# Performance work log

Hardware: AMD Instinct MI355X
Metric: run time of the kernel (lower is better)

The kernel has to match this reference:

```python
import jax, jax.numpy as jnp
import numpy as np

N = 50000      # nodes
E = 800000     # edges
D = 128        # input feature dim
H = 8          # heads
C = 16         # out_channels per head (H*C == D, concat output width == D)
SLOPE = 0.2    # PyG GATConv leaky_relu negative slope


def gat_layer(x, src, dst, W, a_src, a_dst, b):
    # linear transform, shared for src/dst (PyG GATConv with int in_channels)
    h = (x @ W).reshape(N, H, C)                      # [N,H,C]
    alpha_src = jnp.einsum('nhc,hc->nh', h, a_src)    # [N,H]
    alpha_dst = jnp.einsum('nhc,hc->nh', h, a_dst)    # [N,H]
    e = jax.nn.leaky_relu(alpha_src[src] + alpha_dst[dst], SLOPE)  # [E,H]
    # segment softmax over edges grouped by destination node
    emax = jax.ops.segment_max(e, dst, num_segments=N)            # [N,H]
    emax = jnp.where(jnp.isfinite(emax), emax, 0.0)               # nodes with no in-edges
    ex = jnp.exp(e - emax[dst])                                   # [E,H]
    denom = jax.ops.segment_sum(ex, dst, num_segments=N)          # [N,H]
    alpha = ex / (denom[dst] + 1e-16)                             # [E,H]
    # weighted scatter-aggregate of source messages
    out = jax.ops.segment_sum(h[src] * alpha[:, :, None], dst, num_segments=N)  # [N,H,C]
    return out.reshape(N, H * C) + b, alpha


def setup_inputs() -> dict:
    key = jax.random.key(0)
    ks = jax.random.split(key, 10)
    s = 1.0 / np.sqrt(D)
    return {
        'x': jax.random.normal(ks[0], (N, D), dtype=jnp.float32),
        'W1': jax.random.normal(ks[1], (D, H * C), dtype=jnp.float32) * s,
        'a_src1': jax.random.normal(ks[2], (H, C), dtype=jnp.float32) * s,
        'a_dst1': jax.random.normal(ks[3], (H, C), dtype=jnp.float32) * s,
        'b1': jnp.zeros((H * C,), dtype=jnp.float32),
        'W2': jax.random.normal(ks[4], (H * C, H * C), dtype=jnp.float32) * s,
        'a_src2': jax.random.normal(ks[5], (H, C), dtype=jnp.float32) * s,
        'a_dst2': jax.random.normal(ks[6], (H, C), dtype=jnp.float32) * s,
        'b2': jnp.zeros((H * C,), dtype=jnp.float32),
        'edge_index': jax.random.randint(ks[7], (2, E), 0, N, dtype=jnp.int64),
    }


def reference(x, W1, a_src1, a_dst1, b1, W2, a_src2, a_dst2, b2, edge_index):
    src, dst = edge_index[0], edge_index[1]
    x1, alpha1 = gat_layer(x, src, dst, W1, a_src1, a_dst1, b1)
    x2, alpha2 = gat_layer(x1, src, dst, W2, a_src2, a_dst2, b2)
    # matches torch forward: (x, attention_weights per layer)
    return x2, alpha1, alpha2
```

## Files before the change

kernel.cpp:

```cpp
#include <hip/hip_runtime.h>
#include <hip/hip_fp16.h>

#define NN 50000
#define NE 800000
#define SLOPE 0.2f
#define SCAN_B 196
#define ECAP 64

typedef _Float16 half8 __attribute__((ext_vector_type(8)));
typedef float f32x4 __attribute__((ext_vector_type(4)));
typedef unsigned int u32x4 __attribute__((ext_vector_type(4)));

__device__ __forceinline__ float lrelu(float v) { return v >= 0.f ? v : SLOPE * v; }
__device__ __forceinline__ unsigned int f2u(float f) {
    unsigned int b = __float_as_uint(f);
    return (b & 0x80000000u) ? ~b : (b | 0x80000000u);
}
__device__ __forceinline__ float u2f(unsigned int u) {
    return __uint_as_float((u & 0x80000000u) ? (u & 0x7fffffffu) : ~u);
}

__global__ __launch_bounds__(256) void prep_all(
    const float* __restrict__ W1, const float* __restrict__ as1, const float* __restrict__ ad1,
    __half* __restrict__ WT1,
    const float* __restrict__ W2, const float* __restrict__ as2, const float* __restrict__ ad2,
    __half* __restrict__ WT2,
    int* __restrict__ counts, unsigned int* __restrict__ gm1, unsigned int* __restrict__ gm2)
{
    const int t0 = blockIdx.x * 256 + threadIdx.x;
    const int stride = gridDim.x * 256;
    for (int i = t0; i < NN; i += stride) counts[i] = 0;
    if (t0 < 8) { gm1[t0] = f2u(-1e30f); gm2[t0] = f2u(-1e30f); }
    #pragma unroll
    for (int layer = 0; layer < 2; ++layer) {
        const float* W = layer ? W2 : W1;
        const float* as_ = layer ? as2 : as1;
        const float* ad_ = layer ? ad2 : ad1;
        __half* WT = layer ? WT2 : WT1;
        for (int idx = t0; idx < 1024; idx += stride) {
            const int k = idx >> 3, h = idx & 7;
            float s1 = 0.f, s2 = 0.f;
            #pragma unroll
            for (int c = 0; c < 16; ++c) {
                const float w = W[k * 128 + h * 16 + c];
                s1 += w * as_[h * 16 + c];
                s2 += w * ad_[h * 16 + c];
            }
            WT[(size_t)(128 + h) * 128 + k] = (__half)s1;
            WT[(size_t)(136 + h) * 128 + k] = (__half)s2;
        }
        for (int idx = t0; idx < 16384; idx += stride) {
            const int k = idx >> 7, c = idx & 127;
            WT[(size_t)c * 128 + k] = (__half)W[idx];
        }
    }
}

template<bool F32IN>
__global__ __launch_bounds__(256) void mfma_gemm(
    const void* __restrict__ Xin, const __half* __restrict__ WT,
    __half* __restrict__ H16, float* __restrict__ asrc, float* __restrict__ adst,
    unsigned int* __restrict__ gmaxE)
{
    __shared__ __half WTs[144 * 136];
    __shared__ unsigned int smax[8];
    const int t = threadIdx.x;
    const int lane = t & 63;
    const int w = t >> 6;
    const int r16 = lane & 15;
    const int g = lane >> 4;
    const int rowStrip = blockIdx.x * 64 + w * 16;
    const int rowm = min(rowStrip + r16, NN - 1);

    #pragma unroll
    for (int k = 0; k < 9; ++k) {
        const int flat = (t + k * 256) * 8;
        const int row = flat >> 7, col = flat & 127;
        *(half8*)&WTs[row * 136 + col] = *(const half8*)&WT[flat];
    }
    if (t < 8) smax[t] = f2u(-1e30f);

    half8 afr[4];
    if constexpr (F32IN) {
        const float* xr = (const float*)Xin + (size_t)rowm * 128;
        #pragma unroll
        for (int ks = 0; ks < 4; ++ks) {
            const int k0 = ks * 32 + 8 * g;
            const float4 p = *(const float4*)&xr[k0];
            const float4 q = *(const float4*)&xr[k0 + 4];
            half8 a;
            a[0] = (_Float16)p.x; a[1] = (_Float16)p.y; a[2] = (_Float16)p.z; a[3] = (_Float16)p.w;
            a[4] = (_Float16)q.x; a[5] = (_Float16)q.y; a[6] = (_Float16)q.z; a[7] = (_Float16)q.w;
            afr[ks] = a;
        }
    } else {
        const __half* xr = (const __half*)Xin + (size_t)rowm * 128;
        #pragma unroll
        for (int ks = 0; ks < 4; ++ks) {
            afr[ks] = *(const half8*)&xr[ks * 32 + 8 * g];
        }
    }
    __syncthreads();

    for (int ct = 0; ct < 9; ++ct) {
        f32x4 acc = {0.f, 0.f, 0.f, 0.f};
        const __half* wrow = &WTs[(ct * 16 + r16) * 136 + 8 * g];
        #pragma unroll
        for (int ks = 0; ks < 4; ++ks) {
            const half8 b = *(const half8*)&wrow[ks * 32];
            acc = __builtin_amdgcn_mfma_f32_16x16x32_f16(afr[ks], b, acc, 0, 0, 0);
        }
        if (ct < 8) {
            #pragma unroll
            for (int rr = 0; rr < 4; ++rr) {
                const int r = rowStrip + 4 * g + rr;
                if (r < NN) H16[(size_t)r * 128 + ct * 16 + r16] = (__half)acc[rr];
            }
        } else {
            float lmax = fmaxf(fmaxf(acc[0], acc[1]), fmaxf(acc[2], acc[3]));
            #pragma unroll
            for (int rr = 0; rr < 4; ++rr) {
                const int r = rowStrip + 4 * g + rr;
                if (r < NN) {
                    if (r16 < 8) asrc[(size_t)r * 8 + r16] = acc[rr];
                    else         adst[(size_t)r * 8 + (r16 - 8)] = acc[rr];
                }
            }
            lmax = fmaxf(lmax, __shfl_xor(lmax, 16));
            lmax = fmaxf(lmax, __shfl_xor(lmax, 32));
            if (g == 0 && r16 < 8) atomicMax(&smax[r16], f2u(lmax));
        }
    }
    __syncthreads();
    if (t < 8) atomicMax(&gmaxE[t], smax[t]);
}

__global__ __launch_bounds__(256) void hist_rank(
    const int* __restrict__ dst, int* __restrict__ counts, int* __restrict__ rank) {
    int e = blockIdx.x * 256 + threadIdx.x;
    if (e >= NE) return;
    int d = dst[e];
    if ((unsigned)d >= NN) d = 0;
    rank[e] = atomicAdd(&counts[d], 1);
}

__global__ __launch_bounds__(256) void block_sum(const int* __restrict__ counts,
                                                 int* __restrict__ bsum) {
    __shared__ int red[256];
    int t = threadIdx.x, i = blockIdx.x * 256 + t;
    red[t] = (i < NN) ? counts[i] : 0;
    __syncthreads();
    for (int s = 128; s > 0; s >>= 1) {
        if (t < s) red[t] += red[t + s];
        __syncthreads();
    }
    if (t == 0) bsum[blockIdx.x] = red[0];
}

__global__ __launch_bounds__(256) void scan_bsum(const int* __restrict__ bsum,
                                                 int* __restrict__ boff) {
    __shared__ int sh[256];
    int t = threadIdx.x;
    int v = (t < SCAN_B) ? bsum[t] : 0;
    sh[t] = v;
    __syncthreads();
    for (int d = 1; d < 256; d <<= 1) {
        int u = (t >= d) ? sh[t - d] : 0;
        __syncthreads();
        sh[t] += u;
        __syncthreads();
    }
    if (t < SCAN_B) boff[t] = sh[t] - v;
}

__global__ __launch_bounds__(256) void scan_final(
    const int* __restrict__ counts, const int* __restrict__ boff,
    int* __restrict__ off)
{
    __shared__ int sh[256];
    int t = threadIdx.x, i = blockIdx.x * 256 + t;
    int v = (i < NN) ? counts[i] : 0;
    sh[t] = v;
    __syncthreads();
    for (int d = 1; d < 256; d <<= 1) {
        int u = (t >= d) ? sh[t - d] : 0;
        __syncthreads();
        sh[t] += u;
        __syncthreads();
    }
    if (i < NN) {
        int o = boff[blockIdx.x] + sh[t] - v;
        off[i] = o;
        if (i == NN - 1) off[NN] = o + v;
    }
}

__global__ __launch_bounds__(256) void place_csr(
    const int* __restrict__ src, const int* __restrict__ dst,
    const int* __restrict__ rank, const int* __restrict__ off,
    int2* __restrict__ csrES) {
    int e = blockIdx.x * 256 + threadIdx.x;
    if (e >= NE) return;
    int s = src[e], d = dst[e];
    if ((unsigned)s >= NN) s = 0;
    if ((unsigned)d >= NN) d = 0;
    int pos = off[d] + rank[e];
    unsigned long long v = ((unsigned long long)(unsigned)s << 32) | (unsigned)e;
    __builtin_nontemporal_store(v, (unsigned long long*)&csrES[pos]);
}

__device__ __forceinline__ void gather_fma(
    const __half* __restrict__ H16, int sk, int ql, float pm,
    float4& accA, float4& accB)
{
    float4 raw = *(const float4*)&H16[(size_t)sk * 128 + ql * 8];
    const __half2* ph = (const __half2*)&raw;
    const float2 f0 = __half22float2(ph[0]);
    const float2 f1 = __half22float2(ph[1]);
    const float2 f2 = __half22float2(ph[2]);
    const float2 f3 = __half22float2(ph[3]);
    accA.x = fmaf(f0.x, pm, accA.x);
    accA.y = fmaf(f0.y, pm, accA.y);
    accA.z = fmaf(f1.x, pm, accA.z);
    accA.w = fmaf(f1.y, pm, accA.w);
    accB.x = fmaf(f2.x, pm, accB.x);
    accB.y = fmaf(f2.y, pm, accB.y);
    accB.z = fmaf(f3.x, pm, accB.z);
    accB.w = fmaf(f3.y, pm, accB.w);
}

template<typename OT, bool NTOUT>
__global__ __launch_bounds__(256) void node_fused(
    const int* __restrict__ off, const int2* __restrict__ csrES,
    const float* __restrict__ asrc, const float* __restrict__ adst,
    const unsigned int* __restrict__ gmaxE,
    const __half* __restrict__ H16, const float* __restrict__ bias,
    float* __restrict__ alpha, OT* __restrict__ out)
{
    __shared__ float pcache[4][ECAP * 8];
    __shared__ int2  scache[4][ECAP];
    const int w = threadIdx.x >> 6;
    int wid = (blockIdx.x * 256 + threadIdx.x) >> 6;
    if (wid >= NN) return;
    const int lane = threadIdx.x & 63;
    const int n = wid;
    const int p0 = off[n], p1 = off[n + 1];
    const int deg = p1 - p0;
    const int h = lane & 7;
    const int el = lane >> 3;
    const float ad = adst[n * 8 + h];
    const float M = lrelu(u2f(gmaxE[h]) + ad);

    const int q  = lane >> 4;
    const int ql = lane & 15;
    const int hq = ql >> 1;

    float l = 0.f;
    float4 accA = make_float4(0.f, 0.f, 0.f, 0.f);
    float4 accB = make_float4(0.f, 0.f, 0.f, 0.f);

    if (deg > 0) {
        const int pEnd = p1 - 1;
        int2  es = csrES[min(p0 + el, pEnd)];
        float av = asrc[(size_t)es.y * 8 + h];
        for (int base = 0; base < deg; base += 8) {
            int2 es_nx = csrES[min(p0 + base + 8 + el, pEnd)];
            const int i = base + el;
            const int s = es.y;
            float p = 0.f;
            if (i < deg) {
                p = __expf(lrelu(av + ad) - M);
                l += p;
                if (i < ECAP) {
                    pcache[w][i * 8 + h] = p;
                    if (h == 0) scache[w][i] = es;
                }
            }
            const int cnt = min(8, deg - base);
            {
                const int kc = min(q, cnt - 1);
                const float pk = __shfl(p, kc * 8 + hq);
                const int   sk = __shfl(s, kc * 8);
                const float pm = (q < cnt) ? pk : 0.f;
                gather_fma(H16, sk, ql, pm, accA, accB);
            }
            if (cnt > 4) {
                const int kw = 4 + q;
                const int kc = min(kw, cnt - 1);
                const float pk = __shfl(p, kc * 8 + hq);
                const int   sk = __shfl(s, kc * 8);
                const float pm = (kw < cnt) ? pk : 0.f;
                gather_fma(H16, sk, ql, pm, accA, accB);
            }
            av = asrc[(size_t)es_nx.y * 8 + h];
            es = es_nx;
        }
    }
    l += __shfl_xor(l, 8);
    l += __shfl_xor(l, 16);
    l += __shfl_xor(l, 32);
    const float inv = 1.f / (l + 1e-16f);

    for (int i = el; i < deg && i < ECAP; i += 8) {
        int2 es = scache[w][i];
        __builtin_nontemporal_store(pcache[w][i * 8 + h] * inv,
                                    &alpha[(size_t)es.x * 8 + h]);
    }
    for (int i = ECAP + el; i < deg; i += 8) {
        int2 es = csrES[p0 + i];
        float v = lrelu(asrc[es.y * 8 + h] + ad);
        __builtin_nontemporal_store(__expf(v - M) * inv,
                                    &alpha[(size_t)es.x * 8 + h]);
    }

    const float invH = __shfl(inv, hq);
    accA.x += __shfl_xor(accA.x, 16); accA.x += __shfl_xor(accA.x, 32);
    accA.y += __shfl_xor(accA.y, 16); accA.y += __shfl_xor(accA.y, 32);
    accA.z += __shfl_xor(accA.z, 16); accA.z += __shfl_xor(accA.z, 32);
    accA.w += __shfl_xor(accA.w, 16); accA.w += __shfl_xor(accA.w, 32);
    accB.x += __shfl_xor(accB.x, 16); accB.x += __shfl_xor(accB.x, 32);
    accB.y += __shfl_xor(accB.y, 16); accB.y += __shfl_xor(accB.y, 32);
    accB.z += __shfl_xor(accB.z, 16); accB.z += __shfl_xor(accB.z, 32);
    accB.w += __shfl_xor(accB.w, 16); accB.w += __shfl_xor(accB.w, 32);
    if (q == 0) {
        const float4 bva = *(const float4*)&bias[ql * 8];
        const float4 bvb = *(const float4*)&bias[ql * 8 + 4];
        const float o0 = accA.x * invH + bva.x, o1 = accA.y * invH + bva.y;
        const float o2 = accA.z * invH + bva.z, o3 = accA.w * invH + bva.w;
        const float o4 = accB.x * invH + bvb.x, o5 = accB.y * invH + bvb.y;
        const float o6 = accB.z * invH + bvb.z, o7 = accB.w * invH + bvb.w;
        if constexpr (sizeof(OT) == 4) {
            if constexpr (NTOUT) {
                f32x4 oa = {o0, o1, o2, o3}, ob = {o4, o5, o6, o7};
                __builtin_nontemporal_store(oa, (f32x4*)&out[(size_t)n * 128 + ql * 8]);
                __builtin_nontemporal_store(ob, (f32x4*)&out[(size_t)n * 128 + ql * 8 + 4]);
            } else {
                float4 oa = {o0, o1, o2, o3}, ob = {o4, o5, o6, o7};
                *(float4*)&out[(size_t)n * 128 + ql * 8]     = oa;
                *(float4*)&out[(size_t)n * 128 + ql * 8 + 4] = ob;
            }
        } else {
            __half2 p0h = __floats2half2_rn(o0, o1);
            __half2 p1h = __floats2half2_rn(o2, o3);
            __half2 p2h = __floats2half2_rn(o4, o5);
            __half2 p3h = __floats2half2_rn(o6, o7);
            u32x4 pk = {*(unsigned*)&p0h, *(unsigned*)&p1h, *(unsigned*)&p2h, *(unsigned*)&p3h};
            if constexpr (NTOUT) {
                __builtin_nontemporal_store(pk, (u32x4*)&out[(size_t)n * 128 + ql * 8]);
            } else {
                *(u32x4*)&out[(size_t)n * 128 + ql * 8] = pk;
            }
        }
    }
}

extern "C" void kernel_launch(void* const* d_in, const int* in_sizes, int n_in,
                              void* d_out, int out_size, void* d_ws, size_t ws_size,
                              hipStream_t stream)
{
    const float* x   = (const float*)d_in[0];
    const float* W1  = (const float*)d_in[1];
    const float* as1 = (const float*)d_in[2];
    const float* ad1 = (const float*)d_in[3];
    const float* b1  = (const float*)d_in[4];
    const float* W2  = (const float*)d_in[5];
    const float* as2 = (const float*)d_in[6];
    const float* ad2 = (const float*)d_in[7];
    const float* b2  = (const float*)d_in[8];
    const int*   ei  = (const int*)d_in[9];
    const int* srcp = ei;
    const int* dstp = ei + NE;

    float* outx   = (float*)d_out;
    float* alpha1 = outx + (size_t)NN * 128;
    float* alpha2 = alpha1 + (size_t)NE * 8;

    __half* h16 = (__half*)d_ws;
    __half* x1h = h16 + (size_t)NN * 128;
    __half* wt1 = x1h + (size_t)NN * 128;
    __half* wt2 = wt1 + (size_t)144 * 128;
    float* asrc = (float*)(wt2 + (size_t)144 * 128);
    float* adst = asrc + (size_t)NN * 8;
    int* counts = (int*)(adst + (size_t)NN * 8);
    int* off    = counts + NN;
    int* rank   = off + NN + 1;
    int2* csrES = (int2*)(rank + NE);
    int* bsum   = (int*)(csrES + NE);
    int* boff   = bsum + SCAN_B;
    unsigned int* gm1 = (unsigned int*)(boff + SCAN_B);
    unsigned int* gm2 = gm1 + 8;

    int gemmGrid = (NN + 63) / 64;
    int nodeGrid = (NN + 3) / 4;
    int edgeGrid = (NE + 255) / 256;

    prep_all<<<SCAN_B, 256, 0, stream>>>(W1, as1, ad1, wt1, W2, as2, ad2, wt2, counts, gm1, gm2);
    hist_rank<<<edgeGrid, 256, 0, stream>>>(dstp, counts, rank);
    block_sum<<<SCAN_B, 256, 0, stream>>>(counts, bsum);
    scan_bsum<<<1, 256, 0, stream>>>(bsum, boff);
    scan_final<<<SCAN_B, 256, 0, stream>>>(counts, boff, off);
    place_csr<<<edgeGrid, 256, 0, stream>>>(srcp, dstp, rank, off, csrES);

    mfma_gemm<true><<<gemmGrid, 256, 0, stream>>>(x, wt1, h16, asrc, adst, gm1);
    node_fused<__half, false><<<nodeGrid, 256, 0, stream>>>(off, csrES, asrc, adst, gm1, h16, b1, alpha1, x1h);

    mfma_gemm<false><<<gemmGrid, 256, 0, stream>>>(x1h, wt2, h16, asrc, adst, gm2);
    node_fused<float, true><<<nodeGrid, 256, 0, stream>>>(off, csrES, asrc, adst, gm2, h16, b2, alpha2, outx);
}
```

Baseline: 215.2 us.

## Fuse CSR placement into first GEMM and unroll edge loop by sixteen

The separate place_csr kernel is removed, and its scatter of (src, edge) pairs into CSR order moves into the first MFMA GEMM kernel. Each GEMM block handles 1024 edges, loading them before the matrix work and storing them after it, which saves one launch and overlaps the scatter with compute. The node aggregation loop is also unrolled to process two groups of 8 edges per iteration, putting more independent gathers in flight. The cost is higher register pressure in both kernels. Coverage depends on the GEMM grid (782 blocks × 1024 edges) being large enough to cover all 800000 edges.

```diff
diff --git a/kernel.cpp b/kernel.cpp
--- a/kernel.cpp
+++ b/kernel.cpp
@@ -56,11 +56,14 @@
     }
 }
 
-template<bool F32IN>
+template<bool F32IN, bool DOPLACE>
 __global__ __launch_bounds__(256) void mfma_gemm(
     const void* __restrict__ Xin, const __half* __restrict__ WT,
     __half* __restrict__ H16, float* __restrict__ asrc, float* __restrict__ adst,
-    unsigned int* __restrict__ gmaxE)
+    unsigned int* __restrict__ gmaxE,
+    const int* __restrict__ srcA, const int* __restrict__ dstA,
+    const int* __restrict__ rank, const int* __restrict__ offA,
+    int2* __restrict__ csrES)
 {
     __shared__ __half WTs[144 * 136];
     __shared__ unsigned int smax[8];
@@ -79,6 +82,24 @@
         *(half8*)&WTs[row * 136 + col] = *(const half8*)&WT[flat];
     }
     if (t < 8) smax[t] = f2u(-1e30f);
+
+    int ppos[DOPLACE ? 4 : 1];
+    unsigned long long pval[DOPLACE ? 4 : 1];
+    if constexpr (DOPLACE) {
+        const int eBase = blockIdx.x * 1024;
+        #pragma unroll
+        for (int k = 0; k < 4; ++k) {
+            const int e = eBase + k * 256 + t;
+            ppos[k] = -1;
+            if (e < NE) {
+                int s = srcA[e], d = dstA[e];
+                if ((unsigned)s >= NN) s = 0;
+                if ((unsigned)d >= NN) d = 0;
+                ppos[k] = offA[d] + rank[e];
+                pval[k] = ((unsigned long long)(unsigned)s << 32) | (unsigned)e;
+            }
+        }
+    }
 
     half8 afr[4];
     if constexpr (F32IN) {
@@ -131,6 +152,15 @@
             if (g == 0 && r16 < 8) atomicMax(&smax[r16], f2u(lmax));
         }
     }
+
+    if constexpr (DOPLACE) {
+        #pragma unroll
+        for (int k = 0; k < 4; ++k) {
+            if (ppos[k] >= 0) {
+                __builtin_nontemporal_store(pval[k], (unsigned long long*)&csrES[ppos[k]]);
+            }
+        }
+    }
     __syncthreads();
     if (t < 8) atomicMax(&gmaxE[t], smax[t]);
 }
@@ -193,20 +223,6 @@
         off[i] = o;
         if (i == NN - 1) off[NN] = o + v;
     }
-}
-
-__global__ __launch_bounds__(256) void place_csr(
-    const int* __restrict__ src, const int* __restrict__ dst,
-    const int* __restrict__ rank, const int* __restrict__ off,
-    int2* __restrict__ csrES) {
-    int e = blockIdx.x * 256 + threadIdx.x;
-    if (e >= NE) return;
-    int s = src[e], d = dst[e];
-    if ((unsigned)s >= NN) s = 0;
-    if ((unsigned)d >= NN) d = 0;
-    int pos = off[d] + rank[e];
-    unsigned long long v = ((unsigned long long)(unsigned)s << 32) | (unsigned)e;
-    __builtin_nontemporal_store(v, (unsigned long long*)&csrES[pos]);
 }
 
 __device__ __forceinline__ void gather_fma(
@@ -261,39 +277,62 @@
 
     if (deg > 0) {
         const int pEnd = p1 - 1;
-        int2  es = csrES[min(p0 + el, pEnd)];
-        float av = asrc[(size_t)es.y * 8 + h];
-        for (int base = 0; base < deg; base += 8) {
-            int2 es_nx = csrES[min(p0 + base + 8 + el, pEnd)];
-            const int i = base + el;
-            const int s = es.y;
-            float p = 0.f;
-            if (i < deg) {
-                p = __expf(lrelu(av + ad) - M);
-                l += p;
-                if (i < ECAP) {
-                    pcache[w][i * 8 + h] = p;
-                    if (h == 0) scache[w][i] = es;
+        int2  esA = csrES[min(p0 + el, pEnd)];
+        int2  esB = csrES[min(p0 + 8 + el, pEnd)];
+        float avA = asrc[(size_t)esA.y * 8 + h];
+        float avB = asrc[(size_t)esB.y * 8 + h];
+        for (int base = 0; base < deg; base += 16) {
+            int2 esA_nx = csrES[min(p0 + base + 16 + el, pEnd)];
+            int2 esB_nx = csrES[min(p0 + base + 24 + el, pEnd)];
+            const int iA = base + el, iB = base + 8 + el;
+            const int sA = esA.y, sB = esB.y;
+            float pA = 0.f, pB = 0.f;
+            if (iA < deg) {
+                pA = __expf(lrelu(avA + ad) - M);
+                l += pA;
+                if (iA < ECAP) {
+                    pcache[w][iA * 8 + h] = pA;
+                    if (h == 0) scache[w][iA] = esA;
                 }
             }
-            const int cnt = min(8, deg - base);
+            if (iB < deg) {
+                pB = __expf(lrelu(avB + ad) - M);
+                l += pB;
+                if (iB < ECAP) {
+                    pcache[w][iB * 8 + h] = pB;
+                    if (h == 0) scache[w][iB] = esB;
+                }
+            }
+            const int cntA = min(8, deg - base);
+            const int cntB = min(8, max(0, deg - base - 8));
             {
-                const int kc = min(q, cnt - 1);
-                const float pk = __shfl(p, kc * 8 + hq);
-                const int   sk = __shfl(s, kc * 8);
-                const float pm = (q < cnt) ? pk : 0.f;
-                gather_fma(H16, sk, ql, pm, accA, accB);
-            }
-            if (cnt > 4) {
-                const int kw = 4 + q;
-                const int kc = min(kw, cnt - 1);
-                const float pk = __shfl(p, kc * 8 + hq);
-                const int   sk = __shfl(s, kc * 8);
-                const float pm = (kw < cnt) ? pk : 0.f;
-                gather_fma(H16, sk, ql, pm, accA, accB);
-            }
-            av = asrc[(size_t)es_nx.y * 8 + h];
-            es = es_nx;
+                const int kc = min(q, cntA - 1);
+                const float pk = __shfl(pA, kc * 8 + hq);
+                const int   sk = __shfl(sA, kc * 8);
+                gather_fma(H16, sk, ql, (q < cntA) ? pk : 0.f, accA, accB);
+            }
+            if (cntA > 4) {
+                const int kw = 4 + q, kc = min(kw, cntA - 1);
+                const float pk = __shfl(pA, kc * 8 + hq);
+                const int   sk = __shfl(sA, kc * 8);
+                gather_fma(H16, sk, ql, (kw < cntA) ? pk : 0.f, accA, accB);
+            }
+            if (cntB > 0) {
+                const int kc = min(q, cntB - 1);
+                const float pk = __shfl(pB, kc * 8 + hq);
+                const int   sk = __shfl(sB, kc * 8);
+                gather_fma(H16, sk, ql, (q < cntB) ? pk : 0.f, accA, accB);
+            }
+            if (cntB > 4) {
+                const int kw = 4 + q, kc = min(kw, cntB - 1);
+                const float pk = __shfl(pB, kc * 8 + hq);
+                const int   sk = __shfl(sB, kc * 8);
+                gather_fma(H16, sk, ql, (kw < cntB) ? pk : 0.f, accA, accB);
+            }
+            avA = asrc[(size_t)esA_nx.y * 8 + h];
+            avB = asrc[(size_t)esB_nx.y * 8 + h];
+            esA = esA_nx;
+            esB = esB_nx;
         }
     }
     l += __shfl_xor(l, 8);
@@ -399,11 +438,12 @@
     block_sum<<<SCAN_B, 256, 0, stream>>>(counts, bsum);
     scan_bsum<<<1, 256, 0, stream>>>(bsum, boff);
     scan_final<<<SCAN_B, 256, 0, stream>>>(counts, boff, off);
-    place_csr<<<edgeGrid, 256, 0, stream>>>(srcp, dstp, rank, off, csrES);
-
-    mfma_gemm<true><<<gemmGrid, 256, 0, stream>>>(x, wt1, h16, asrc, adst, gm1);
+
+    mfma_gemm<true, true><<<gemmGrid, 256, 0, stream>>>(
+        x, wt1, h16, asrc, adst, gm1, srcp, dstp, rank, off, csrES);
     node_fused<__half, false><<<nodeGrid, 256, 0, stream>>>(off, csrES, asrc, adst, gm1, h16, b1, alpha1, x1h);
 
-    mfma_gemm<false><<<gemmGrid, 256, 0, stream>>>(x1h, wt2, h16, asrc, adst, gm2);
+    mfma_gemm<false, false><<<gemmGrid, 256, 0, stream>>>(
+        x1h, wt2, h16, asrc, adst, gm2, nullptr, nullptr, nullptr, nullptr, nullptr);
     node_fused<float, true><<<nodeGrid, 256, 0, stream>>>(off, csrES, asrc, adst, gm2, h16, b2, alpha2, outx);
 }
```

Result: faster. 206.3 us, median of 2 (-4.1%).
